# Performance work log

Measured on AMD Instinct MI355X. Metric: run time of the kernel, lower is better.

The kernel has to match this reference:

```python
import jax, jax.numpy as jnp
import numpy as np

B, T, F, H, OUT, L = 4096, 336, 12, 50, 1, 3


def _lstm_layer(x_tbf, W_ih, W_hh, b_ih, b_hh):
    """PyTorch-semantics LSTM layer. x_tbf: [T,B,in]; returns [T,B,H]."""
    Hh = W_hh.shape[1]
    Bsz = x_tbf.shape[1]
    # precompute input projection for all timesteps: [T,B,4H]
    xz = jnp.einsum('tbf,gf->tbg', x_tbf, W_ih) + (b_ih + b_hh)

    def step(carry, xz_t):
        h, c = carry
        z = xz_t + h @ W_hh.T  # [B,4H]
        i, f, g, o = jnp.split(z, 4, axis=-1)  # PyTorch gate order i,f,g,o
        c = jax.nn.sigmoid(f) * c + jax.nn.sigmoid(i) * jnp.tanh(g)
        h = jax.nn.sigmoid(o) * jnp.tanh(c)
        return (h, c), h

    h0 = jnp.zeros((Bsz, Hh), x_tbf.dtype)
    c0 = jnp.zeros((Bsz, Hh), x_tbf.dtype)
    _, hs = jax.lax.scan(step, (h0, c0), xz)
    return hs


def setup_inputs() -> dict:
    key = jax.random.key(0)
    ks = jax.random.split(key, 16)
    s = 1.0 / np.sqrt(H)  # PyTorch LSTM init scale
    inp = {"x": jax.random.normal(ks[0], (B, T, F), dtype=jnp.float32)}
    in_sizes = [F, H, H]
    k = 1
    for l in range(L):
        inp[f"W_ih_{l}"] = jax.random.uniform(ks[k], (4 * H, in_sizes[l]), jnp.float32, -s, s); k += 1
        inp[f"W_hh_{l}"] = jax.random.uniform(ks[k], (4 * H, H), jnp.float32, -s, s); k += 1
        inp[f"b_ih_{l}"] = jax.random.uniform(ks[k], (4 * H,), jnp.float32, -s, s); k += 1
        inp[f"b_hh_{l}"] = jax.random.uniform(ks[k], (4 * H,), jnp.float32, -s, s); k += 1
    inp["W_lin"] = jax.random.uniform(ks[13], (OUT, H), jnp.float32, -s, s)
    inp["b_lin"] = jax.random.uniform(ks[14], (OUT,), jnp.float32, -s, s)
    return inp


def reference(x, W_ih_0, W_hh_0, b_ih_0, b_hh_0,
              W_ih_1, W_hh_1, b_ih_1, b_hh_1,
              W_ih_2, W_hh_2, b_ih_2, b_hh_2,
              W_lin, b_lin):
    h = jnp.transpose(x, (1, 0, 2))  # [T,B,F] time-major for scan
    params = [(W_ih_0, W_hh_0, b_ih_0, b_hh_0),
              (W_ih_1, W_hh_1, b_ih_1, b_hh_1),
              (W_ih_2, W_hh_2, b_ih_2, b_hh_2)]
    for W_ih, W_hh, bi, bh in params:
        h = _lstm_layer(h, W_ih, W_hh, bi, bh)  # [T,B,H]
    last = h[-1]  # out[:, -1, :] in batch_first layout
    return last @ W_lin.T + b_lin  # [B,OUT]
```

## Files before the change

### kernel.cpp

```cpp
#include <hip/hip_runtime.h>


#define Bsz 4096
#define Tt  336
#define BT  16
#define NTH 1024

typedef _Float16 half8 __attribute__((ext_vector_type(8)));
typedef float    floatx4 __attribute__((ext_vector_type(4)));

struct __align__(16) SMem {
  _Float16 act0[2][BT * 64];
  _Float16 act1[2][BT * 128];
  _Float16 act2[2][BT * 128];
};

__device__ __forceinline__ int offA0(int n, int L) {
  return n * 64 + ((((L >> 3) ^ n) & 7) << 3) + (L & 7);
}
__device__ __forceinline__ int offA12(int n, int L) {
  return n * 128 + ((((L >> 3) ^ n) & 15) << 3) + (L & 7);
}

__device__ __forceinline__ float lstm_cell(floatx4 z, float& c) {
  float ei = __builtin_amdgcn_exp2f(z[0]);
  float ef = __builtin_amdgcn_exp2f(z[1]);
  float eg = __builtin_amdgcn_exp2f(z[2]);
  float eo = __builtin_amdgcn_exp2f(z[3]);
  float ig = __builtin_amdgcn_rcpf(1.f + ei);
  float fg = __builtin_amdgcn_rcpf(1.f + ef);
  float rg = __builtin_amdgcn_rcpf(1.f + eg);
  float og = __builtin_amdgcn_rcpf(1.f + eo);
  float gg = 1.f - 2.f * rg;
  c = fg * c + ig * gg;
  float ec = __builtin_amdgcn_exp2f(2.885390082f * c);
  float rc = __builtin_amdgcn_rcpf(1.f + ec);
  return og * (1.f - 2.f * rc);
}

__device__ __forceinline__ half8 wfrag(const float* __restrict__ Wih,
                                       const float* __restrict__ Whh,
                                       int lenih, int bound, int R, int k0) {
  half8 r = {};
  int u = R >> 2, g = R & 3;
  float sc = (g == 2) ? 2.885390082f : -1.442695041f;
  if (u < 50) {
    int row = g * 50 + u;
#pragma unroll
    for (int j = 0; j < 8; ++j) {
      int k = k0 + j;
      float v = 0.f;
      if (k < bound)           v = Wih[row * lenih + k];
      else if (k < bound + 50) v = Whh[row * 50 + (k - bound)];
      r[j] = (_Float16)(sc * v);
    }
  }
  return r;
}

__device__ __forceinline__ void wait_all(int* prog, unsigned mask, int need, int lane) {
  bool mine = (lane < 16) && ((mask >> lane) & 1u);
  while (true) {
    int v = mine ? __hip_atomic_load(&prog[lane & 15], __ATOMIC_RELAXED,
                                     __HIP_MEMORY_SCOPE_WORKGROUP)
                 : 0x7fffffff;
    if (__all(v >= need)) break;
    __builtin_amdgcn_s_sleep(1);
  }
  asm volatile("" ::: "memory");
}
__device__ __forceinline__ void store_prog(int* slot, int val, int lane) {
  asm volatile("s_waitcnt lgkmcnt(0)" ::: "memory");
  if (lane == 0)
    __hip_atomic_store(slot, val, __ATOMIC_RELAXED, __HIP_MEMORY_SCOPE_WORKGROUP);
}

#define MFMA(a, b, acc) __builtin_amdgcn_mfma_f32_16x16x32_f16((a), (b), (acc), 0, 0, 0)

#define MASK_L0   0x200Fu
#define MASK_L1   0x40F0u
#define MASK_L2   0x9F00u
#define MASK_L01  0x60FFu
#define MASK_L12  0xDFF0u

__global__ __launch_bounds__(NTH, 4)
void lstm_mfma_kernel(const float* __restrict__ x,
                      const float* __restrict__ Wih0, const float* __restrict__ Whh0,
                      const float* __restrict__ bih0, const float* __restrict__ bhh0,
                      const float* __restrict__ Wih1, const float* __restrict__ Whh1,
                      const float* __restrict__ bih1, const float* __restrict__ bhh1,
                      const float* __restrict__ Wih2, const float* __restrict__ Whh2,
                      const float* __restrict__ bih2, const float* __restrict__ bhh2,
                      const float* __restrict__ Wlin, const float* __restrict__ blin,
                      float* __restrict__ out) {
  __shared__ SMem sm;
  __shared__ int wrprog[16];
  __shared__ int rdprog[16];
  const int tid  = threadIdx.x;
  const int blk  = blockIdx.x;
  const int lane = tid & 63;
  const int w    = tid >> 6;
  const int n    = lane & 15;
  const int q    = lane >> 4;

  {
    int* zp = (int*)&sm;
    for (int i = tid; i < (int)(sizeof(SMem) / 4); i += NTH) zp[i] = 0;
  }
  if (tid < 16) { wrprog[tid] = 0; rdprog[tid] = 0; }

  int Lw, nc, mm3[3] = {0, 0, 0};
  switch (w) {
    case 0:  Lw = 0; nc = 3; mm3[0] = 0;  mm3[1] = 1;  mm3[2] = 2;  break;
    case 1:  Lw = 0; nc = 2; mm3[0] = 3;  mm3[1] = 4;               break;
    case 2:  Lw = 0; nc = 3; mm3[0] = 5;  mm3[1] = 6;  mm3[2] = 7;  break;
    case 3:  Lw = 0; nc = 2; mm3[0] = 8;  mm3[1] = 9;               break;
    case 4:  Lw = 1; nc = 2; mm3[0] = 0;  mm3[1] = 1;               break;
    case 5:  Lw = 1; nc = 3; mm3[0] = 2;  mm3[1] = 3;  mm3[2] = 4;  break;
    case 6:  Lw = 1; nc = 2; mm3[0] = 5;  mm3[1] = 6;               break;
    case 7:  Lw = 1; nc = 3; mm3[0] = 7;  mm3[1] = 8;  mm3[2] = 9;  break;
    case 8:  Lw = 2; nc = 3; mm3[0] = 0;  mm3[1] = 1;  mm3[2] = 2;  break;
    case 9:  Lw = 2; nc = 2; mm3[0] = 3;  mm3[1] = 4;               break;
    case 10: Lw = 2; nc = 2; mm3[0] = 5;  mm3[1] = 6;               break;
    case 11: Lw = 2; nc = 2; mm3[0] = 7;  mm3[1] = 8;               break;
    case 12: Lw = 2; nc = 2; mm3[0] = 9;  mm3[1] = 10;              break;
    case 13: Lw = 0; nc = 3; mm3[0] = 10; mm3[1] = 11; mm3[2] = 12; break;
    case 14: Lw = 1; nc = 3; mm3[0] = 10; mm3[1] = 11; mm3[2] = 12; break;
    default: Lw = 2; nc = 2; mm3[0] = 11; mm3[1] = 12;              break;
  }
  const float* Wih = (Lw == 0) ? Wih0 : ((Lw == 1) ? Wih1 : Wih2);
  const float* Whh = (Lw == 0) ? Whh0 : ((Lw == 1) ? Whh1 : Whh2);
  const float* bih = (Lw == 0) ? bih0 : ((Lw == 1) ? bih1 : bih2);
  const float* bhh = (Lw == 0) ? bhh0 : ((Lw == 1) ? bhh1 : bhh2);
  const int lenih = (Lw == 0) ? 12 : 50;
  const int nkc   = (Lw == 0) ? 2 : 4;

  half8  af[3][4];
  floatx4 bia[3];
  float  cst[3] = {0.f, 0.f, 0.f};
  int    woA[3], woB[3];
  bool   uokk[3];
#pragma unroll
  for (int i = 0; i < 3; ++i) {
    bia[i] = (floatx4){0, 0, 0, 0};
#pragma unroll
    for (int kc = 0; kc < 4; ++kc) af[i][kc] = (half8){};
    int m = mm3[i];
    int u = 4 * m + q;
    int uc = (u < 50) ? u : 49;
    uokk[i] = (i < nc) && (u < 50);
    if (Lw == 0) { woA[i] = offA0 (n, 12 + uc); woB[i] = offA12(n, uc); }
    else         { woA[i] = offA12(n, 50 + uc); woB[i] = offA12(n, uc); }
    if (i < nc) {
      int R = 16 * m + n;
#pragma unroll
      for (int kc = 0; kc < 4; ++kc)
        if (kc < nkc)
          af[i][kc] = wfrag(Wih, Whh, lenih, lenih, R, kc * 32 + q * 8);
      if (u < 50) {
#pragma unroll
        for (int g = 0; g < 4; ++g) {
          float sc = (g == 2) ? 2.885390082f : -1.442695041f;
          bia[i][g] = sc * (bih[g * 50 + u] + bhh[g * 50 + u]);
        }
      }
    }
  }

  const int ro0[2] = { offA0(n, q * 8), offA0(n, 32 + q * 8) };
  const int ro1[4] = { offA12(n, q * 8),      offA12(n, 32 + q * 8),
                       offA12(n, 64 + q * 8), offA12(n, 96 + q * 8) };

  const int sr = (tid < 192) ? tid / 12 : 0;
  const int sf = (tid < 192) ? tid - sr * 12 : 0;
  const int sxo = offA0(sr, sf);
  const float* xp = x + ((size_t)(blk * BT + sr) * Tt) * 12 + sf;
  float xnext = 0.f;

  __syncthreads();
  if (tid < 192) {
    sm.act0[0][sxo] = (_Float16)xp[0];
    xnext = xp[12];
  }
  __syncthreads();

#define TICK(p, TAU, CHK)                                                   \
  {                                                                         \
    if (Lw == 0) {                                                          \
      if (!(CHK) || (TAU) <= 335) {                                         \
        wait_all(wrprog, MASK_L0, (TAU), lane);                             \
        half8 b0 = *(const half8*)&sm.act0[p][ro0[0]];                      \
        half8 b1 = *(const half8*)&sm.act0[p][ro0[1]];                      \
        store_prog(&rdprog[w], (TAU) + 1, lane);                            \
        float hv[3];                                                        \
        for (int i = 0; i < 3; ++i) if (i < nc) {                           \
          floatx4 z = bia[i];                                               \
          z = MFMA(af[i][0], b0, z);                                        \
          z = MFMA(af[i][1], b1, z);                                        \
          hv[i] = lstm_cell(z, cst[i]);                                     \
        }                                                                   \
        wait_all(rdprog, MASK_L01, (TAU), lane);                            \
        if (tid < 192 && (TAU) + 1 < Tt)                                    \
          sm.act0[1 - (p)][sxo] = (_Float16)xnext;                          \
        for (int i = 0; i < 3; ++i) if (uokk[i]) {                          \
          _Float16 hh = (_Float16)hv[i];                                    \
          sm.act0[1 - (p)][woA[i]] = hh;                                    \
          sm.act1[1 - (p)][woB[i]] = hh;                                    \
        }                                                                   \
        store_prog(&wrprog[w], (TAU) + 1, lane);                            \
        if (tid < 192)                                                      \
          xnext = ((TAU) + 2 < Tt) ? xp[((TAU) + 2) * 12] : 0.f;            \
      } else {                                                              \
        store_prog(&rdprog[w], (TAU) + 1, lane);                            \
        store_prog(&wrprog[w], (TAU) + 1, lane);                            \
      }                                                                     \
    } else if (Lw == 1) {                                                   \
      if (!(CHK) || ((TAU) >= 1 && (TAU) <= 336)) {                         \
        wait_all(wrprog, MASK_L01, (TAU), lane);                            \
        half8 b0 = *(const half8*)&sm.act1[p][ro1[0]];                      \
        half8 b1 = *(const half8*)&sm.act1[p][ro1[1]];                      \
        half8 b2 = *(const half8*)&sm.act1[p][ro1[2]];                      \
        half8 b3 = *(const half8*)&sm.act1[p][ro1[3]];                      \
        store_prog(&rdprog[w], (TAU) + 1, lane);                            \
        float hv[3];                                                        \
        for (int i = 0; i < 3; ++i) if (i < nc) {                           \
          floatx4 z = bia[i];                                               \
          z = MFMA(af[i][0], b0, z);                                        \
          z = MFMA(af[i][1], b1, z);                                        \
          z = MFMA(af[i][2], b2, z);                                        \
          z = MFMA(af[i][3], b3, z);                                        \
          hv[i] = lstm_cell(z, cst[i]);                                     \
        }                                                                   \
        wait_all(rdprog, MASK_L12, (TAU), lane);                            \
        for (int i = 0; i < 3; ++i) if (uokk[i]) {                          \
          _Float16 hh = (_Float16)hv[i];                                    \
          sm.act1[1 - (p)][woA[i]] = hh;                                    \
          sm.act2[1 - (p)][woB[i]] = hh;                                    \
        }                                                                   \
        store_prog(&wrprog[w], (TAU) + 1, lane);                            \
      } else {                                                              \
        store_prog(&rdprog[w], (TAU) + 1, lane);                            \
        store_prog(&wrprog[w], (TAU) + 1, lane);                            \
      }                                                                     \
    } else {                                                                \
      if (!(CHK) || ((TAU) >= 2)) {                                         \
        wait_all(wrprog, MASK_L12, (TAU), lane);                            \
        half8 b0 = *(const half8*)&sm.act2[p][ro1[0]];                      \
        half8 b1 = *(const half8*)&sm.act2[p][ro1[1]];                      \
        half8 b2 = *(const half8*)&sm.act2[p][ro1[2]];                      \
        half8 b3 = *(const half8*)&sm.act2[p][ro1[3]];                      \
        store_prog(&rdprog[w], (TAU) + 1, lane);                            \
        float hv[3];                                                        \
        for (int i = 0; i < 3; ++i) if (i < nc) {                           \
          floatx4 z = bia[i];                                               \
          z = MFMA(af[i][0], b0, z);                                        \
          z = MFMA(af[i][1], b1, z);                                        \
          z = MFMA(af[i][2], b2, z);                                        \
          z = MFMA(af[i][3], b3, z);                                        \
          hv[i] = lstm_cell(z, cst[i]);                                     \
        }                                                                   \
        wait_all(rdprog, MASK_L2, (TAU), lane);                             \
        for (int i = 0; i < 3; ++i) if (uokk[i])                            \
          sm.act2[1 - (p)][woA[i]] = (_Float16)hv[i];                       \
        store_prog(&wrprog[w], (TAU) + 1, lane);                            \
      } else {                                                              \
        store_prog(&rdprog[w], (TAU) + 1, lane);                            \
        store_prog(&wrprog[w], (TAU) + 1, lane);                            \
      }                                                                     \
    }                                                                       \
  }

  TICK(0, 0, 1)
  TICK(1, 1, 1)
#pragma unroll 1
  for (int t = 2; t < Tt; t += 2) {
    TICK(0, t, 0)
    TICK(1, t + 1, 0)
  }
  TICK(0, 336, 1)
  TICK(1, 337, 1)
#undef TICK

  __syncthreads();

  if (tid < BT) {
    float s = blin[0];
    for (int uu = 0; uu < 50; ++uu)
      s += Wlin[uu] * (float)sm.act2[0][offA12(tid, 50 + uu)];
    out[blk * BT + tid] = s;
  }
}

extern "C" void kernel_launch(void* const* d_in, const int* in_sizes, int n_in,
                              void* d_out, int out_size, void* d_ws, size_t ws_size,
                              hipStream_t stream) {
  const float* x    = (const float*)d_in[0];
  const float* Wih0 = (const float*)d_in[1];
  const float* Whh0 = (const float*)d_in[2];
  const float* bih0 = (const float*)d_in[3];
  const float* bhh0 = (const float*)d_in[4];
  const float* Wih1 = (const float*)d_in[5];
  const float* Whh1 = (const float*)d_in[6];
  const float* bih1 = (const float*)d_in[7];
  const float* bhh1 = (const float*)d_in[8];
  const float* Wih2 = (const float*)d_in[9];
  const float* Whh2 = (const float*)d_in[10];
  const float* bih2 = (const float*)d_in[11];
  const float* bhh2 = (const float*)d_in[12];
  const float* Wlin = (const float*)d_in[13];
  const float* blin = (const float*)d_in[14];
  float* outp = (float*)d_out;

  dim3 grid(Bsz / BT);
  dim3 block(NTH);
  lstm_mfma_kernel<<<grid, block, 0, stream>>>(
      x, Wih0, Whh0, bih0, bhh0, Wih1, Whh1, bih1, bhh1,
      Wih2, Whh2, bih2, bhh2, Wlin, blin, outp);
}
```

Measured before the change: 492.8 us.

## Replace per-wave progress-counter spin waits with one workgroup barrier per tick

Removes the LDS progress counters (wrprog/rdprog) and their spin-wait/atomic-store handshakes between layer waves. Each tick now ends with a single s_waitcnt plus s_barrier, and hidden-state writes go straight into the other buffer of the double buffer. The x prefetch is moved to the start of each tick and deepened to two steps ahead. This cuts polling and atomic traffic but forces all 16 waves to lockstep, so no wave can run ahead of slower ones.

```diff
diff --git a/kernel.cpp b/kernel.cpp
--- a/kernel.cpp
+++ b/kernel.cpp
@@ -20,6 +20,10 @@
 }
 __device__ __forceinline__ int offA12(int n, int L) {
   return n * 128 + ((((L >> 3) ^ n) & 15) << 3) + (L & 7);
+}
+
+__device__ __forceinline__ void barrier_lgkm() {
+  asm volatile("s_waitcnt lgkmcnt(0)\n\ts_barrier" ::: "memory");
 }
 
 __device__ __forceinline__ float lstm_cell(floatx4 z, float& c) {
@@ -58,30 +62,7 @@
   return r;
 }
 
-__device__ __forceinline__ void wait_all(int* prog, unsigned mask, int need, int lane) {
-  bool mine = (lane < 16) && ((mask >> lane) & 1u);
-  while (true) {
-    int v = mine ? __hip_atomic_load(&prog[lane & 15], __ATOMIC_RELAXED,
-                                     __HIP_MEMORY_SCOPE_WORKGROUP)
-                 : 0x7fffffff;
-    if (__all(v >= need)) break;
-    __builtin_amdgcn_s_sleep(1);
-  }
-  asm volatile("" ::: "memory");
-}
-__device__ __forceinline__ void store_prog(int* slot, int val, int lane) {
-  asm volatile("s_waitcnt lgkmcnt(0)" ::: "memory");
-  if (lane == 0)
-    __hip_atomic_store(slot, val, __ATOMIC_RELAXED, __HIP_MEMORY_SCOPE_WORKGROUP);
-}
-
 #define MFMA(a, b, acc) __builtin_amdgcn_mfma_f32_16x16x32_f16((a), (b), (acc), 0, 0, 0)
-
-#define MASK_L0   0x200Fu
-#define MASK_L1   0x40F0u
-#define MASK_L2   0x9F00u
-#define MASK_L01  0x60FFu
-#define MASK_L12  0xDFF0u
 
 __global__ __launch_bounds__(NTH, 4)
 void lstm_mfma_kernel(const float* __restrict__ x,
@@ -94,8 +75,6 @@
                       const float* __restrict__ Wlin, const float* __restrict__ blin,
                       float* __restrict__ out) {
   __shared__ SMem sm;
-  __shared__ int wrprog[16];
-  __shared__ int rdprog[16];
   const int tid  = threadIdx.x;
   const int blk  = blockIdx.x;
   const int lane = tid & 63;
@@ -107,7 +86,6 @@
     int* zp = (int*)&sm;
     for (int i = tid; i < (int)(sizeof(SMem) / 4); i += NTH) zp[i] = 0;
   }
-  if (tid < 16) { wrprog[tid] = 0; rdprog[tid] = 0; }
 
   int Lw, nc, mm3[3] = {0, 0, 0};
   switch (w) {
@@ -175,99 +153,73 @@
   const int sf = (tid < 192) ? tid - sr * 12 : 0;
   const int sxo = offA0(sr, sf);
   const float* xp = x + ((size_t)(blk * BT + sr) * Tt) * 12 + sf;
-  float xnext = 0.f;
+  float xn1 = 0.f, xn2 = 0.f;
 
   __syncthreads();
   if (tid < 192) {
     sm.act0[0][sxo] = (_Float16)xp[0];
-    xnext = xp[12];
+    xn1 = xp[12];
+    xn2 = xp[24];
   }
   __syncthreads();
 
 #define TICK(p, TAU, CHK)                                                   \
   {                                                                         \
+    if (tid < 192) {                                                        \
+      if ((TAU) + 1 < Tt) sm.act0[1 - (p)][sxo] = (_Float16)xn1;            \
+      xn1 = xn2;                                                            \
+      xn2 = ((TAU) + 3 < Tt) ? xp[((TAU) + 3) * 12] : 0.f;                  \
+    }                                                                       \
     if (Lw == 0) {                                                          \
       if (!(CHK) || (TAU) <= 335) {                                         \
-        wait_all(wrprog, MASK_L0, (TAU), lane);                             \
         half8 b0 = *(const half8*)&sm.act0[p][ro0[0]];                      \
         half8 b1 = *(const half8*)&sm.act0[p][ro0[1]];                      \
-        store_prog(&rdprog[w], (TAU) + 1, lane);                            \
-        float hv[3];                                                        \
         for (int i = 0; i < 3; ++i) if (i < nc) {                           \
           floatx4 z = bia[i];                                               \
           z = MFMA(af[i][0], b0, z);                                        \
           z = MFMA(af[i][1], b1, z);                                        \
-          hv[i] = lstm_cell(z, cst[i]);                                     \
+          float h = lstm_cell(z, cst[i]);                                   \
+          _Float16 hh = (_Float16)h;                                        \
+          if (uokk[i]) { sm.act0[1 - (p)][woA[i]] = hh;                     \
+                         sm.act1[1 - (p)][woB[i]] = hh; }                   \
         }                                                                   \
-        wait_all(rdprog, MASK_L01, (TAU), lane);                            \
-        if (tid < 192 && (TAU) + 1 < Tt)                                    \
-          sm.act0[1 - (p)][sxo] = (_Float16)xnext;                          \
-        for (int i = 0; i < 3; ++i) if (uokk[i]) {                          \
-          _Float16 hh = (_Float16)hv[i];                                    \
-          sm.act0[1 - (p)][woA[i]] = hh;                                    \
-          sm.act1[1 - (p)][woB[i]] = hh;                                    \
-        }                                                                   \
-        store_prog(&wrprog[w], (TAU) + 1, lane);                            \
-        if (tid < 192)                                                      \
-          xnext = ((TAU) + 2 < Tt) ? xp[((TAU) + 2) * 12] : 0.f;            \
-      } else {                                                              \
-        store_prog(&rdprog[w], (TAU) + 1, lane);                            \
-        store_prog(&wrprog[w], (TAU) + 1, lane);                            \
       }                                                                     \
     } else if (Lw == 1) {                                                   \
       if (!(CHK) || ((TAU) >= 1 && (TAU) <= 336)) {                         \
-        wait_all(wrprog, MASK_L01, (TAU), lane);                            \
         half8 b0 = *(const half8*)&sm.act1[p][ro1[0]];                      \
         half8 b1 = *(const half8*)&sm.act1[p][ro1[1]];                      \
         half8 b2 = *(const half8*)&sm.act1[p][ro1[2]];                      \
         half8 b3 = *(const half8*)&sm.act1[p][ro1[3]];                      \
-        store_prog(&rdprog[w], (TAU) + 1, lane);                            \
-        float hv[3];                                                        \
         for (int i = 0; i < 3; ++i) if (i < nc) {                           \
           floatx4 z = bia[i];                                               \
           z = MFMA(af[i][0], b0, z);                                        \
           z = MFMA(af[i][1], b1, z);                                        \
           z = MFMA(af[i][2], b2, z);                                        \
           z = MFMA(af[i][3], b3, z);                                        \
-          hv[i] = lstm_cell(z, cst[i]);                                     \
+          float h = lstm_cell(z, cst[i]);                                   \
+          _Float16 hh = (_Float16)h;                                        \
+          if (uokk[i]) { sm.act1[1 - (p)][woA[i]] = hh;                     \
+                         sm.act2[1 - (p)][woB[i]] = hh; }                   \
         }                                                                   \
-        wait_all(rdprog, MASK_L12, (TAU), lane);                            \
-        for (int i = 0; i < 3; ++i) if (uokk[i]) {                          \
-          _Float16 hh = (_Float16)hv[i];                                    \
-          sm.act1[1 - (p)][woA[i]] = hh;                                    \
-          sm.act2[1 - (p)][woB[i]] = hh;                                    \
-        }                                                                   \
-        store_prog(&wrprog[w], (TAU) + 1, lane);                            \
-      } else {                                                              \
-        store_prog(&rdprog[w], (TAU) + 1, lane);                            \
-        store_prog(&wrprog[w], (TAU) + 1, lane);                            \
       }                                                                     \
     } else {                                                                \
       if (!(CHK) || ((TAU) >= 2)) {                                         \
-        wait_all(wrprog, MASK_L12, (TAU), lane);                            \
         half8 b0 = *(const half8*)&sm.act2[p][ro1[0]];                      \
         half8 b1 = *(const half8*)&sm.act2[p][ro1[1]];                      \
         half8 b2 = *(const half8*)&sm.act2[p][ro1[2]];                      \
         half8 b3 = *(const half8*)&sm.act2[p][ro1[3]];                      \
-        store_prog(&rdprog[w], (TAU) + 1, lane);                            \
-        float hv[3];                                                        \
         for (int i = 0; i < 3; ++i) if (i < nc) {                           \
           floatx4 z = bia[i];                                               \
           z = MFMA(af[i][0], b0, z);                                        \
           z = MFMA(af[i][1], b1, z);                                        \
           z = MFMA(af[i][2], b2, z);                                        \
           z = MFMA(af[i][3], b3, z);                                        \
-          hv[i] = lstm_cell(z, cst[i]);                                     \
+          float h = lstm_cell(z, cst[i]);                                   \
+          if (uokk[i]) sm.act2[1 - (p)][woA[i]] = (_Float16)h;              \
         }                                                                   \
-        wait_all(rdprog, MASK_L2, (TAU), lane);                             \
-        for (int i = 0; i < 3; ++i) if (uokk[i])                            \
-          sm.act2[1 - (p)][woA[i]] = (_Float16)hv[i];                       \
-        store_prog(&wrprog[w], (TAU) + 1, lane);                            \
-      } else {                                                              \
-        store_prog(&rdprog[w], (TAU) + 1, lane);                            \
-        store_prog(&wrprog[w], (TAU) + 1, lane);                            \
       }                                                                     \
     }                                                                       \
+    barrier_lgkm();                                                         \
   }
 
   TICK(0, 0, 1)
```

New measurement: 415.6 us. 15.7% less time.
